# Optimization experiments

Hardware: AMD Instinct MI355X
Metric: run time of the kernel (lower is better)

## Reference

```python
import jax, jax.numpy as jnp
import numpy as np

B_, N, C, H = 512, 49, 256, 8
DH = C // H            # 32
RB, NRF = 8, 32
NWIN = B_ // RB        # 64
DC = 64                # class_token_dim
TC = C + 2 * DC        # 384
WS = 7
SCALE = DH ** -0.5


def _rel_pos_index():
    ch = np.arange(WS)
    coords = np.stack(np.meshgrid(ch, ch, indexing='ij')).reshape(2, -1)  # [2,49]
    rel = (coords[:, :, None] - coords[:, None, :]).transpose(1, 2, 0)    # [49,49,2]
    rel[..., 0] += WS - 1
    rel[..., 1] += WS - 1
    rel[..., 0] *= 2 * WS - 1
    return jnp.asarray(rel.sum(-1).reshape(-1))  # [49*49]


def _ln(x, axes, eps=1e-5):
    m = x.mean(axes, keepdims=True)
    v = x.var(axes, keepdims=True)
    return (x - m) * jax.lax.rsqrt(v + eps)


def setup_inputs() -> dict:
    key = jax.random.key(0)
    ks = jax.random.split(key, 20)
    def w(i, shape, s=0.02):
        return jax.random.normal(ks[i], shape, jnp.float32) * s
    return dict(
        x=w(0, (B_, N, C), 1.0),
        x_ref=w(1, (RB, NRF, C), 1.0),
        depth_token=w(2, (B_, N, DC), 1.0),
        seg_token=w(3, (B_, N, DC), 1.0),
        qkv_w=w(4, (C, 3 * C)), qkv_b=jnp.zeros(3 * C, jnp.float32),
        proj_w=w(5, (C, C)), proj_b=jnp.zeros(C, jnp.float32),
        rel_bias=w(6, ((2 * WS - 1) ** 2, H)),
        diff_mu=w(7, (1, 1, C), 1.0), diff_logsigma=w(8, (1, 1, C)),
        ref_qk_w=w(9, (C, 2 * C)), ref_qk_b=jnp.zeros(2 * C, jnp.float32),
        conv_w=w(10, (H, H, 3, 3), 0.1), conv_b=jnp.zeros(H, jnp.float32),
        q_norm_w=jnp.ones(C, jnp.float32), q_norm_b=jnp.zeros(C, jnp.float32),
        q_proj_w=w(11, (C, C)), q_proj_b=jnp.zeros(C, jnp.float32),
        cls_dth_q_w=w(12, (DC, DC)), cls_dth_q_b=jnp.zeros(DC, jnp.float32),
        cls_seg_q_w=w(13, (DC, DC)), cls_seg_q_b=jnp.zeros(DC, jnp.float32),
        global_k_w=w(14, (TC, TC)), global_k_b=jnp.zeros(TC, jnp.float32),
        global_v_w=w(15, (TC, TC)), global_v_b=jnp.zeros(TC, jnp.float32),
        proj_dth_w=w(16, (DC, DC)), proj_dth_b=jnp.zeros(DC, jnp.float32),
    )


def reference(x, x_ref, depth_token, seg_token, qkv_w, qkv_b, proj_w, proj_b,
              rel_bias, diff_mu, diff_logsigma, ref_qk_w, ref_qk_b, conv_w, conv_b,
              q_norm_w, q_norm_b, q_proj_w, q_proj_b, cls_dth_q_w, cls_dth_q_b,
              cls_seg_q_w, cls_seg_q_b, global_k_w, global_k_b, global_v_w,
              global_v_b, proj_dth_w, proj_dth_b):
    # qkv: [B_,N,3C] -> q,k,v each [B_,H,N,DH]
    qkv = (x @ qkv_w + qkv_b).reshape(B_, N, 3, H, DH).transpose(2, 0, 3, 1, 4)
    q, k, v = qkv[0], qkv[1], qkv[2]

    # ---- group attention (ref branch) ----
    ref_qk = (x_ref @ ref_qk_w + ref_qk_b).reshape(RB, NRF, 2, C).transpose(2, 0, 1, 3)
    ref_q, ref_v = ref_qk[0], ref_qk[1]                       # [RB,NRF,C]
    ref_q = diff_mu + jnp.exp(diff_logsigma) * ref_q
    ref_q = ref_q.reshape(RB, NRF, H, DH).transpose(0, 2, 1, 3)  # [RB,H,NRF,DH]
    ref_v = ref_v.reshape(RB, NRF, H, DH).transpose(0, 2, 1, 3)

    qs = (q * SCALE).reshape(RB, NWIN, H, N, DH)
    # scores against shared (per-image) ref keys; avoids materializing repeated K
    ref_attn = jnp.einsum('rwhnd,rhfd->rhwnf', qs, ref_q)     # [RB,H,NWIN,N,NRF]
    ref_attn_r = ref_attn.reshape(RB, H, NWIN * N, NRF)
    # 3-step diffusion: conv2d over heads-as-channels + LN(no affine) + gelu, residual
    for _ in range(3):
        u = jax.lax.conv_general_dilated(
            ref_attn_r, conv_w, (1, 1), 'SAME',
            dimension_numbers=('NCHW', 'OIHW', 'NCHW')) + conv_b[None, :, None, None]
        u = jax.nn.gelu(_ln(u, (-2, -1)), approximate=False)
        ref_attn_r = ref_attn_r + u
    ref_attn = jax.nn.softmax(ref_attn_r.reshape(RB, H, NWIN, N, NRF), axis=-1)
    q_new = jnp.einsum('rhwnf,rhfd->rwnhd', ref_attn, ref_v).reshape(B_, N, C)
    q_sc = q.transpose(0, 2, 1, 3).reshape(B_, N, C)          # unscaled shortcut
    q_new = (_ln(q_new + q_sc, (-1,)) * q_norm_w + q_norm_b) @ q_proj_w + q_proj_b + q_sc
    q_new = q_new.reshape(B_, N, H, DH).transpose(0, 2, 1, 3) * SCALE

    # ---- window attention with relative position bias ----
    bias = rel_bias[_rel_pos_index()].reshape(N, N, H).transpose(2, 0, 1)  # [H,N,N]
    attn = jax.nn.softmax(jnp.einsum('bhnd,bhmd->bhnm', q_new, k) + bias[None], axis=-1)
    out = jnp.einsum('bhnm,bhmd->bnhd', attn, v).reshape(B_, N, C)
    out = out @ proj_w + proj_b

    # ---- class-token global attention ----
    dch = DC // H   # 8
    tdh = TC // H   # 48
    depth_q = (depth_token @ cls_dth_q_w + cls_dth_q_b).reshape(B_, N, H, dch).transpose(0, 2, 1, 3) * SCALE
    seg_q = (seg_token @ cls_seg_q_w + cls_seg_q_b).reshape(B_, N, H, dch).transpose(0, 2, 1, 3) * SCALE
    t_x = jnp.concatenate([out, depth_token, seg_token], axis=-1)  # [B_,N,TC]
    t_k = (t_x @ global_k_w + global_k_b).reshape(B_, N, H, tdh).transpose(0, 2, 1, 3)
    t_v = (t_x @ global_v_w + global_v_b).reshape(B_, N, H, tdh).transpose(0, 2, 1, 3)

    d_attn = jax.nn.softmax(jnp.einsum('bhnc,bhnt->bhct', depth_q, t_k), axis=-1)
    d_tok = jnp.einsum('bhct,bhnt->bhcn', d_attn, t_v).reshape(B_, DC, N).transpose(0, 2, 1)
    d_tok = d_tok @ proj_dth_w + proj_dth_b
    s_attn = jax.nn.softmax(jnp.einsum('bhnc,bhnt->bhct', seg_q, t_k), axis=-1)
    s_tok = jnp.einsum('bhct,bhnt->bhcn', s_attn, t_v).reshape(B_, DC, N).transpose(0, 2, 1)
    s_tok = s_tok @ proj_dth_w + proj_dth_b  # NOTE: original uses proj_dth for seg too
    return out, d_tok, s_tok
```

## Files before the change

### kernel.cpp

```cpp
#include <hip/hip_runtime.h>
#include <hip/hip_bf16.h>

typedef __hip_bfloat16 bf16;
typedef short s16x8 __attribute__((ext_vector_type(8)));
typedef float f32x4 __attribute__((ext_vector_type(4)));
union V16 { uint4 u4; s16x8 s8; unsigned u[4]; unsigned short s[8]; };

static __device__ __forceinline__ float b2f(bf16 v){ return __bfloat162float(v); }
static __device__ __forceinline__ bf16  f2b(float v){ return __float2bfloat16(v); }
static __device__ __forceinline__ unsigned short f2bs(float x){
    union { float f; unsigned u; } c; c.f = x;
    unsigned r = c.u + 0x7fff + ((c.u >> 16) & 1);
    return (unsigned short)(r >> 16);
}
static __device__ __forceinline__ float bu2f(unsigned short b){
    union { unsigned u; float f; } c; c.u = ((unsigned)b) << 16; return c.f;
}
static __device__ __forceinline__ s16x8 ld16g(const bf16* p){
    V16 u; u.u4 = *(const uint4*)p; return u.s8;
}
static __device__ __forceinline__ void glds16(const void* g, void* l){
    __builtin_amdgcn_global_load_lds(
        (const __attribute__((address_space(1))) unsigned*)g,
        (__attribute__((address_space(3))) unsigned*)l, 16, 0, 0);
}

#define SCALE_T 0.17677669529663687f

__global__ __launch_bounds__(256) void prep_weights(
    const float* __restrict__ qkvw, const float* __restrict__ qpw,
    const float* __restrict__ pw,   const float* __restrict__ gkw,
    const float* __restrict__ gvw,  bf16* __restrict__ Wt)
{
    int idx = blockIdx.x * 256 + threadIdx.x;
    float v;
    if (idx < 196608)      { int j = idx;          int n = j >> 8, k = j & 255; v = qkvw[k * 768 + n]; }
    else if (idx < 262144) { int j = idx - 196608; int n = j >> 8, k = j & 255; v = qpw[k * 256 + n]; }
    else if (idx < 327680) { int j = idx - 262144; int n = j >> 8, k = j & 255; v = pw[k * 256 + n]; }
    else if (idx < 475136) { int j = idx - 327680; int n = j / 384, k = j - n * 384; v = gkw[k * 384 + n]; }
    else                   { int j = idx - 475136; int n = j / 384, k = j - n * 384; v = gvw[k * 384 + n]; }
    ((unsigned short*)Wt)[idx] = f2bs(v);
}

__global__ __launch_bounds__(256) void convert_f32_bf16(
    const float* __restrict__ in, bf16* __restrict__ out)
{
    int i = blockIdx.x * 256 + threadIdx.x;
    float4 v = ((const float4*)in)[i];
    ushort4 o;
    o.x = f2bs(v.x); o.y = f2bs(v.y); o.z = f2bs(v.z); o.w = f2bs(v.w);
    ((ushort4*)out)[i] = o;
}

__global__ __launch_bounds__(256) void tok2b_kernel(
    const float* __restrict__ dth, const float* __restrict__ seg,
    bf16* __restrict__ tokb)
{
    int i = blockIdx.x * 256 + threadIdx.x;
    int row = i >> 4, j8 = i & 15;
    const float* src = (j8 < 8) ? (dth + (size_t)row * 64 + j8 * 8)
                                : (seg + (size_t)row * 64 + (j8 - 8) * 8);
    float4 u0 = ((const float4*)src)[0];
    float4 u1 = ((const float4*)src)[1];
    V16 o;
    o.s[0] = f2bs(u0.x); o.s[1] = f2bs(u0.y);
    o.s[2] = f2bs(u0.z); o.s[3] = f2bs(u0.w);
    o.s[4] = f2bs(u1.x); o.s[5] = f2bs(u1.y);
    o.s[6] = f2bs(u1.z); o.s[7] = f2bs(u1.w);
    *(uint4*)(tokb + (size_t)row * 128 + j8 * 8) = o.u4;
}

template<int TOK>
__global__ __launch_bounds__(256, 4) void gemm_bb(
    const bf16* __restrict__ A, int lda, const bf16* __restrict__ A2,
    const bf16* __restrict__ Wt, const float* __restrict__ bias,
    const float* __restrict__ bias2,
    const bf16* __restrict__ addp, int addStride,
    float* __restrict__ outF, bf16* __restrict__ outB, int outStrideB,
    int K, int N, float scale)
{
    __shared__ char lds[2][16384];

    const int tid = threadIdx.x;
    const int wv = tid >> 6, lane = tid & 63;
    const int quad = lane >> 4, l15 = lane & 15;
    const int wr = wv >> 1, wc = wv & 1;

    const int gx = (int)gridDim.x;
    const int nwg = gx * (int)gridDim.y;
    int bid = (int)blockIdx.y * gx + (int)blockIdx.x;
    if ((nwg & 7) == 0) bid = (bid & 7) * (nwg >> 3) + (bid >> 3);
    const int bx = bid % gx, by = bid / gx;
    const int rowBase = by * 128, colBase = bx * 128;

    const int srow = tid >> 2;
    const int kOffE = (((tid & 3) ^ ((srow >> 1) & 3)) << 3);

    const unsigned swz = (unsigned)((quad ^ ((l15 >> 1) & 3)) << 4);
    const unsigned aoff0 = (unsigned)(wr * 4096 + l15 * 64) + swz;
    const unsigned boff0 = (unsigned)(wc * 4096 + l15 * 64) + swz;

    f32x4 acc[4][4];
    #pragma unroll
    for (int m = 0; m < 4; ++m)
        #pragma unroll
        for (int n = 0; n < 4; ++n)
            #pragma unroll
            for (int r = 0; r < 4; ++r) acc[m][n][r] = 0.f;

    auto stage = [&](int sbuf, int kt) {
        char* base = &lds[sbuf][0];
        #pragma unroll
        for (int c = 0; c < 2; ++c)
            glds16(Wt + (size_t)(colBase + c * 64 + srow) * K + (kt + kOffE),
                   base + 8192 + c * 4096 + tid * 16);
        if (!TOK || kt < 256) {
            #pragma unroll
            for (int c = 0; c < 2; ++c)
                glds16(A + (size_t)(rowBase + c * 64 + srow) * lda + (kt + kOffE),
                       base + c * 4096 + tid * 16);
        } else {
            #pragma unroll
            for (int c = 0; c < 2; ++c)
                glds16(A2 + (size_t)(rowBase + c * 64 + srow) * 128 + (kt - 256 + kOffE),
                       base + c * 4096 + tid * 16);
        }
    };

    stage(0, 0);
    __syncthreads();
    int buf = 0;
    for (int kt = 0; kt < K; kt += 32) {
        if (kt + 32 < K) stage(buf ^ 1, kt + 32);
        const char* Ab2 = &lds[buf][0];
        const char* Bb2 = Ab2 + 8192;
        s16x8 af[4], bfr[4];
        #pragma unroll
        for (int m = 0; m < 4; ++m) af[m]  = *(const s16x8*)(Ab2 + aoff0 + m * 1024);
        #pragma unroll
        for (int n = 0; n < 4; ++n) bfr[n] = *(const s16x8*)(Bb2 + boff0 + n * 1024);
        #pragma unroll
        for (int m = 0; m < 4; ++m)
            #pragma unroll
            for (int n = 0; n < 4; ++n)
                acc[m][n] = __builtin_amdgcn_mfma_f32_16x16x32_bf16(af[m], bfr[n], acc[m][n], 0, 0, 0);
        __syncthreads();
        buf ^= 1;
    }

    if (outB) {
        #pragma unroll
        for (int n = 0; n < 4; ++n) {
            int col = colBase + wc * 64 + n * 16 + l15;
            float bb = bias2 ? (col < 384 ? bias[col] : bias2[col - 384]) : bias[col];
            #pragma unroll
            for (int m = 0; m < 4; ++m) {
                #pragma unroll
                for (int r = 0; r < 4; ++r) {
                    int rl = wr * 64 + m * 16 + quad * 4 + r;
                    float v = acc[m][n][r] + bb;
                    if (addp) v += b2f(addp[(size_t)(rowBase + rl) * addStride + col]);
                    v *= scale;
                    if (outF) outF[(size_t)(rowBase + rl) * N + col] = v;
                    int cbyte = (wc * 64 + n * 16 + l15) * 2;
                    int blk = ((cbyte >> 5) ^ ((rl >> 2) & 7)) & 7;
                    *(unsigned short*)((char*)lds + rl * 256 + (blk << 5) + (cbyte & 31)) = f2bs(v);
                }
            }
        }
        __syncthreads();
        #pragma unroll
        for (int i = 0; i < 8; ++i) {
            int lin = i * 256 + tid;
            int rl = lin >> 4, cb = lin & 15;
            int cb2 = ((((cb >> 1) ^ ((rl >> 2) & 7)) & 7) << 1) | (cb & 1);
            uint4 val = *(const uint4*)((const char*)lds + rl * 256 + cb2 * 16);
            *(uint4*)(outB + (size_t)(rowBase + rl) * outStrideB + colBase + cb * 8) = val;
        }
    } else {
        #pragma unroll
        for (int n = 0; n < 4; ++n) {
            int col = colBase + wc * 64 + n * 16 + l15;
            float bb = bias2 ? (col < 384 ? bias[col] : bias2[col - 384]) : bias[col];
            #pragma unroll
            for (int m = 0; m < 4; ++m) {
                #pragma unroll
                for (int r = 0; r < 4; ++r) {
                    int rl = wr * 64 + m * 16 + quad * 4 + r;
                    float v = acc[m][n][r] + bb;
                    if (addp) v += b2f(addp[(size_t)(rowBase + rl) * addStride + col]);
                    v *= scale;
                    if (outF) outF[(size_t)(rowBase + rl) * N + col] = v;
                }
            }
        }
    }
}

template<int AF32, int OF32>
__global__ __launch_bounds__(256) void small64(
    const void* __restrict__ a0, const void* __restrict__ a1,
    const float* __restrict__ w0, const float* __restrict__ w1,
    const float* __restrict__ b0, const float* __restrict__ b1,
    void* __restrict__ o0, void* __restrict__ o1, float scale)
{
    __shared__ unsigned short WT[64 * 72];
    __shared__ float bsh[64];
    const int task = blockIdx.y;
    const void*  A    = task ? a1 : a0;
    const float* W    = task ? w1 : w0;
    const float* bias = task ? b1 : b0;
    void*        outp = task ? o1 : o0;

    int tid = threadIdx.x;
    for (int l = tid; l < 4096; l += 256) {
        int k = l >> 6, n = l & 63;
        WT[n * 72 + k] = f2bs(W[l]);
    }
    if (tid < 64) bsh[tid] = bias[tid];
    __syncthreads();

    const int wv = tid >> 6, lane = tid & 63;
    const int quad = lane >> 4, l15 = lane & 15;
    const int rowBase = blockIdx.x * 64;
    const int arow = rowBase + wv * 16 + l15;

    s16x8 a[2];
    if (AF32) {
        const float* Ar = (const float*)A + (size_t)arow * 64;
        #pragma unroll
        for (int ks = 0; ks < 2; ++ks) {
            float4 u0 = *(const float4*)(Ar + ks * 32 + quad * 8);
            float4 u1 = *(const float4*)(Ar + ks * 32 + quad * 8 + 4);
            V16 o;
            o.s[0] = f2bs(u0.x); o.s[1] = f2bs(u0.y);
            o.s[2] = f2bs(u0.z); o.s[3] = f2bs(u0.w);
            o.s[4] = f2bs(u1.x); o.s[5] = f2bs(u1.y);
            o.s[6] = f2bs(u1.z); o.s[7] = f2bs(u1.w);
            a[ks] = o.s8;
        }
    } else {
        const bf16* Ar = (const bf16*)A + (size_t)arow * 64;
        #pragma unroll
        for (int ks = 0; ks < 2; ++ks)
            a[ks] = ld16g(Ar + ks * 32 + quad * 8);
    }

    f32x4 acc[4];
    #pragma unroll
    for (int n = 0; n < 4; ++n)
        #pragma unroll
        for (int r = 0; r < 4; ++r) acc[n][r] = 0.f;

    #pragma unroll
    for (int ks = 0; ks < 2; ++ks)
        #pragma unroll
        for (int n = 0; n < 4; ++n) {
            s16x8 b = *(const s16x8*)&WT[(n * 16 + l15) * 72 + ks * 32 + quad * 8];
            acc[n] = __builtin_amdgcn_mfma_f32_16x16x32_bf16(a[ks], b, acc[n], 0, 0, 0);
        }

    #pragma unroll
    for (int n = 0; n < 4; ++n) {
        int col = n * 16 + l15;
        float bb = bsh[col];
        #pragma unroll
        for (int r = 0; r < 4; ++r) {
            int row = rowBase + wv * 16 + quad * 4 + r;
            float v = (acc[n][r] + bb) * scale;
            if (OF32) ((float*)outp)[(size_t)row * 64 + col] = v;
            else      ((bf16*)outp)[(size_t)row * 64 + col] = f2b(v);
        }
    }
}

__global__ __launch_bounds__(256) void mfma_gemm(
    const void* __restrict__ A, int a_mode,
    const float* __restrict__ W, const float* __restrict__ bias,
    float* __restrict__ outF, bf16* __restrict__ outB,
    int M, int K, int N, float scale)
{
    __shared__ __hip_bfloat16 Al[64][48];
    __shared__ __hip_bfloat16 Bl[64][48];

    const int tid  = threadIdx.x;
    const int wv   = tid >> 6, lane = tid & 63;
    const int quad = lane >> 4, l15 = lane & 15;
    const int rowBase = blockIdx.y * 64, colBase = blockIdx.x * 64;

    const int am = tid >> 2, ak = (tid & 3) * 8;
    const int bn = tid & 63, bk = (tid >> 6) * 8;

    f32x4 acc[4];
    #pragma unroll
    for (int t = 0; t < 4; ++t)
        #pragma unroll
        for (int r = 0; r < 4; ++r) acc[t][r] = 0.f;

    for (int kt = 0; kt < K; kt += 32) {
        s16x8 sa;
        if (a_mode == 1) {
            const bf16* Ab = (const bf16*)A;
            V16 u; u.u4 = *(const uint4*)(Ab + (size_t)(rowBase + am) * K + kt + ak);
            sa = u.s8;
        } else {
            const float* src = (const float*)A;
            const float4* p = (const float4*)(src + (size_t)(rowBase + am) * K + kt + ak);
            float4 u0 = p[0], u1 = p[1];
            sa[0] = (short)f2bs(u0.x); sa[1] = (short)f2bs(u0.y);
            sa[2] = (short)f2bs(u0.z); sa[3] = (short)f2bs(u0.w);
            sa[4] = (short)f2bs(u1.x); sa[5] = (short)f2bs(u1.y);
            sa[6] = (short)f2bs(u1.z); sa[7] = (short)f2bs(u1.w);
        }
        *(s16x8*)&Al[am][ak] = sa;

        s16x8 sb;
        #pragma unroll
        for (int j = 0; j < 8; ++j)
            sb[j] = (short)f2bs(W[(size_t)(kt + bk + j) * N + colBase + bn]);
        *(s16x8*)&Bl[bn][bk] = sb;

        __syncthreads();

        s16x8 a = *(const s16x8*)&Al[wv * 16 + l15][quad * 8];
        #pragma unroll
        for (int t = 0; t < 4; ++t) {
            s16x8 b = *(const s16x8*)&Bl[t * 16 + l15][quad * 8];
            acc[t] = __builtin_amdgcn_mfma_f32_16x16x32_bf16(a, b, acc[t], 0, 0, 0);
        }
        __syncthreads();
    }

    #pragma unroll
    for (int t = 0; t < 4; ++t) {
        int col = colBase + t * 16 + l15;
        float bb = bias[col];
        #pragma unroll
        for (int r = 0; r < 4; ++r) {
            int row = rowBase + wv * 16 + quad * 4 + r;
            float v = (acc[t][r] + bb) * scale;
            if (outF) outF[(size_t)row * N + col] = v;
            if (outB) outB[(size_t)row * N + col] = f2b(v);
        }
    }
}

__global__ __launch_bounds__(256) void refprep_kernel(
    const float* __restrict__ ref_qk, const float* __restrict__ mu,
    const float* __restrict__ ls, float* __restrict__ ref_q_t,
    float* __restrict__ ref_v_t)
{
    int idx = blockIdx.x * 256 + threadIdx.x;
    int d = idx & 31, f = (idx >> 5) & 31, h = (idx >> 10) & 7, r = idx >> 13;
    int c = h * 32 + d;
    size_t src = (size_t)(r * 32 + f) * 512 + c;
    ref_q_t[idx] = mu[c] + __expf(ls[c]) * ref_qk[src];
    ref_v_t[idx] = ref_qk[src + 256];
}

__global__ __launch_bounds__(256) void refattn_kernel(
    const bf16* __restrict__ qkv, const float* __restrict__ ref_q_t,
    bf16* __restrict__ ref_attn, float* __restrict__ statsA)
{
    int blk = blockIdx.x;
    int tid = threadIdx.x;
    if (blk == 0 && tid < 384) statsA[tid] = 0.f;
    int w = blk & 63, h = (blk >> 6) & 7, r = blk >> 9;
    int b = r * 64 + w;
    __shared__ float qt[49 * 32];
    __shared__ float rq[32 * 33];
    for (int l = tid; l < 1568; l += 256) {
        int n = l >> 5, d = l & 31;
        qt[l] = b2f(qkv[(size_t)(b * 49 + n) * 768 + h * 32 + d]) * SCALE_T;
    }
    for (int l = tid; l < 1024; l += 256) {
        int f = l >> 5, d = l & 31;
        rq[f * 33 + d] = ref_q_t[(size_t)((r * 8 + h) * 32 + f) * 32 + d];
    }
    __syncthreads();
    for (int l = tid; l < 1568; l += 256) {
        int n = l >> 5, f = l & 31;
        float acc = 0.f;
        #pragma unroll
        for (int d2 = 0; d2 < 32; ++d2) acc += qt[n * 32 + d2] * rq[f * 33 + d2];
        ref_attn[(size_t)(((r * 8 + h) * 64 + w) * 49 + n) * 32 + f] = f2b(acc);
    }
}

__global__ __launch_bounds__(256) void conv_kernel(
    const bf16* __restrict__ in, const float* __restrict__ conv_w,
    const float* __restrict__ conv_b, bf16* __restrict__ u,
    float* __restrict__ statsIt)
{
    __shared__ float w_s[576];
    __shared__ float b_s[8];
    __shared__ float red1[4][8], red2[4][8];
    int tid = threadIdx.x;
    for (int l = tid; l < 576; l += 256) w_s[l] = conv_w[l];
    if (tid < 8) b_s[tid] = conv_b[tid];
    __syncthreads();

    int idx = blockIdx.x * 256 + tid;
    int fb = idx & 3;
    int p  = (idx >> 2) % 3136;
    int r  = idx / 12544;
    int f0 = fb * 8;

    float acc[8][8];
    #pragma unroll
    for (int o = 0; o < 8; ++o) {
        float bo = b_s[o];
        #pragma unroll
        for (int f = 0; f < 8; ++f) acc[o][f] = bo;
    }

    for (int i = 0; i < 8; ++i) {
        float ext[3][10];
        #pragma unroll
        for (int dy = 0; dy < 3; ++dy) {
            int pp = p + dy - 1;
            bool pv = (unsigned)pp < 3136u;
            size_t base = ((size_t)((r * 8 + i) * 3136 + (pv ? pp : 0))) * 32 + f0;
            V16 uv;
            uv.u4 = pv ? *(const uint4*)(in + base) : make_uint4(0, 0, 0, 0);
            #pragma unroll
            for (int j = 0; j < 8; ++j) {
                unsigned sh = uv.u[j >> 1];
                unsigned bits = (j & 1) ? (sh & 0xffff0000u) : (sh << 16);
                union { unsigned uu; float fl; } cv; cv.uu = bits;
                ext[dy][j + 1] = cv.fl;
            }
            ext[dy][0] = (pv && f0 > 0)      ? b2f(in[base - 1]) : 0.f;
            ext[dy][9] = (pv && f0 + 8 < 32) ? b2f(in[base + 8]) : 0.f;
        }
        #pragma unroll
        for (int o = 0; o < 8; ++o) {
            #pragma unroll
            for (int ky = 0; ky < 3; ++ky) {
                const float* wp = &w_s[((o * 8 + i) * 3 + ky) * 3];
                float w0 = wp[0], w1 = wp[1], w2 = wp[2];
                #pragma unroll
                for (int f = 0; f < 8; ++f)
                    acc[o][f] += ext[ky][f] * w0 + ext[ky][f + 1] * w1 + ext[ky][f + 2] * w2;
            }
        }
    }

    float so[8], s2o[8];
    #pragma unroll
    for (int o = 0; o < 8; ++o) {
        bf16 ov[8];
        float s = 0.f, s2 = 0.f;
        #pragma unroll
        for (int f = 0; f < 8; ++f) {
            ov[f] = f2b(acc[o][f]);
            s += acc[o][f]; s2 += acc[o][f] * acc[o][f];
        }
        so[o] = s; s2o[o] = s2;
        *(uint4*)(u + ((size_t)((r * 8 + o) * 3136 + p)) * 32 + f0) = *(uint4*)ov;
    }

    #pragma unroll
    for (int o = 0; o < 8; ++o) {
        #pragma unroll
        for (int off = 32; off > 0; off >>= 1) {
            so[o]  += __shfl_xor(so[o],  off);
            s2o[o] += __shfl_xor(s2o[o], off);
        }
    }
    int wv = tid >> 6, lane = tid & 63;
    if (lane == 0) {
        #pragma unroll
        for (int o = 0; o < 8; ++o) { red1[wv][o] = so[o]; red2[wv][o] = s2o[o]; }
    }
    __syncthreads();
    if (tid < 8) {
        float s = red1[0][tid] + red1[1][tid] + red1[2][tid] + red1[3][tid];
        float s2 = red2[0][tid] + red2[1][tid] + red2[2][tid] + red2[3][tid];
        int g = r * 8 + tid;
        atomicAdd(&statsIt[g * 2], s);
        atomicAdd(&statsIt[g * 2 + 1], s2);
    }
}

__global__ __launch_bounds__(256) void lngelu_kernel(
    const bf16* __restrict__ u, const float* __restrict__ statsIt,
    bf16* __restrict__ ref_attn)
{
    int idx8 = blockIdx.x * 256 + threadIdx.x;
    int g = idx8 / 12544;
    size_t base = (size_t)idx8 * 8;
    float sum = statsIt[g * 2], sq = statsIt[g * 2 + 1];
    float mean = sum * (1.f / 100352.f);
    float var  = sq * (1.f / 100352.f) - mean * mean;
    var = fmaxf(var, 0.f);
    float rstd = rsqrtf(var + 1e-5f);
    V16 uv; uv.u4 = *(const uint4*)(u + base);
    V16 rv; rv.u4 = *(const uint4*)(ref_attn + base);
    bf16 outv[8];
    #pragma unroll
    for (int j = 0; j < 8; ++j) {
        unsigned shu = uv.u[j >> 1];
        unsigned shr = rv.u[j >> 1];
        unsigned bu = (j & 1) ? (shu & 0xffff0000u) : (shu << 16);
        unsigned br = (j & 1) ? (shr & 0xffff0000u) : (shr << 16);
        union { unsigned uu; float fl; } cu, cr; cu.uu = bu; cr.uu = br;
        float v = (cu.fl - mean) * rstd;
        float ge = 0.5f * v * (1.f + erff(v * 0.7071067811865476f));
        outv[j] = f2b(cr.fl + ge);
    }
    *(uint4*)(ref_attn + base) = *(uint4*)outv;
}

__global__ __launch_bounds__(256) void qnew_pre_kernel(
    const bf16* __restrict__ qkv, const bf16* __restrict__ ref_attn,
    const float* __restrict__ ref_v_t,
    const float* __restrict__ qnw, const float* __restrict__ qnb,
    bf16* __restrict__ ln_t)
{
    int ww = threadIdx.x >> 6, lane = threadIdx.x & 63;
    int row = blockIdx.x * 4 + ww;
    int b = row / 49, n = row % 49;
    int r = b >> 6, w = b & 63;
    int h = lane >> 3, d0 = (lane & 7) * 4;

    const bf16* la = ref_attn + ((size_t)(((r * 8 + h) * 64 + w) * 49 + n)) * 32 + d0;
    ushort4 lu = *(const ushort4*)la;
    float lg[4] = { bu2f(lu.x), bu2f(lu.y), bu2f(lu.z), bu2f(lu.w) };

    float m = fmaxf(fmaxf(lg[0], lg[1]), fmaxf(lg[2], lg[3]));
    m = fmaxf(m, __shfl_xor(m, 1));
    m = fmaxf(m, __shfl_xor(m, 2));
    m = fmaxf(m, __shfl_xor(m, 4));
    float p[4], s = 0.f;
    #pragma unroll
    for (int j = 0; j < 4; ++j) { p[j] = __expf(lg[j] - m); s += p[j]; }
    s += __shfl_xor(s, 1);
    s += __shfl_xor(s, 2);
    s += __shfl_xor(s, 4);
    float inv = 1.f / s;
    #pragma unroll
    for (int j = 0; j < 4; ++j) p[j] *= inv;

    const float* rv = ref_v_t + ((size_t)(r * 8 + h) * 32) * 32 + d0;
    float y[4] = {0.f, 0.f, 0.f, 0.f};
    #pragma unroll
    for (int f = 0; f < 32; ++f) {
        int src = (lane & 56) | (f >> 2);
        float pf = __shfl(p[f & 3], src);
        float4 rvf = *(const float4*)(rv + f * 32);
        y[0] += pf * rvf.x; y[1] += pf * rvf.y;
        y[2] += pf * rvf.z; y[3] += pf * rvf.w;
    }

    ushort4 qu = *(const ushort4*)(qkv + (size_t)row * 768 + lane * 4);
    float z[4] = { y[0] + bu2f(qu.x), y[1] + bu2f(qu.y),
                   y[2] + bu2f(qu.z), y[3] + bu2f(qu.w) };

    float s1 = z[0] + z[1] + z[2] + z[3];
    #pragma unroll
    for (int off = 1; off < 64; off <<= 1) s1 += __shfl_xor(s1, off);
    float mean = s1 * (1.f / 256.f);
    float zc[4] = { z[0] - mean, z[1] - mean, z[2] - mean, z[3] - mean };
    float s2 = zc[0]*zc[0] + zc[1]*zc[1] + zc[2]*zc[2] + zc[3]*zc[3];
    #pragma unroll
    for (int off = 1; off < 64; off <<= 1) s2 += __shfl_xor(s2, off);
    float rstd = rsqrtf(s2 * (1.f / 256.f) + 1e-5f);

    float4 wv = *(const float4*)(qnw + lane * 4);
    float4 bv = *(const float4*)(qnb + lane * 4);
    bf16 outv[4];
    outv[0] = f2b(zc[0] * rstd * wv.x + bv.x);
    outv[1] = f2b(zc[1] * rstd * wv.y + bv.y);
    outv[2] = f2b(zc[2] * rstd * wv.z + bv.z);
    outv[3] = f2b(zc[3] * rstd * wv.w + bv.w);
    *(ushort4*)(ln_t + (size_t)row * 256 + lane * 4) = *(ushort4*)outv;
}

__global__ __launch_bounds__(256) void winattn_kernel(
    const bf16* __restrict__ qkv, const bf16* __restrict__ q_new,
    const float* __restrict__ rel_bias, bf16* __restrict__ attn_out)
{
    const int wv = threadIdx.x >> 6, lane = threadIdx.x & 63;
    const int quad = lane >> 4, l15 = lane & 15;
    const int b = blockIdx.x >> 1;
    const int h = (blockIdx.x & 1) * 4 + wv;

    __shared__ bf16 lds[4 * 6912];
    bf16* P  = &lds[wv * 6912];
    bf16* vT = P + 4608;

    {
        int m = lane;
        if (m < 49) {
            const bf16* vp = qkv + ((size_t)(b * 49 + m)) * 768 + 512 + h * 32;
            V16 v0, v1, v2, v3;
            v0.u4 = *(const uint4*)(vp);
            v1.u4 = *(const uint4*)(vp + 8);
            v2.u4 = *(const uint4*)(vp + 16);
            v3.u4 = *(const uint4*)(vp + 24);
            #pragma unroll
            for (int d = 0; d < 8; ++d) {
                ((unsigned short*)vT)[d * 72 + m]        = v0.s[d];
                ((unsigned short*)vT)[(d + 8) * 72 + m]  = v1.s[d];
                ((unsigned short*)vT)[(d + 16) * 72 + m] = v2.s[d];
                ((unsigned short*)vT)[(d + 24) * 72 + m] = v3.s[d];
            }
        } else {
            #pragma unroll
            for (int d = 0; d < 32; ++d)
                ((unsigned short*)vT)[d * 72 + m] = 0;
        }
    }

    s16x8 aq[4], bk[4];
    #pragma unroll
    for (int t = 0; t < 4; ++t) {
        int qr = t * 16 + l15; qr = qr > 48 ? 48 : qr;
        aq[t] = ld16g(q_new + ((size_t)(b * 49 + qr)) * 256 + h * 32 + quad * 8);
        bk[t] = ld16g(qkv + ((size_t)(b * 49 + qr)) * 768 + 256 + h * 32 + quad * 8);
    }
    f32x4 S[4][4];
    #pragma unroll
    for (int tn = 0; tn < 4; ++tn)
        #pragma unroll
        for (int tm = 0; tm < 4; ++tm) {
            #pragma unroll
            for (int r = 0; r < 4; ++r) S[tn][tm][r] = 0.f;
            S[tn][tm] = __builtin_amdgcn_mfma_f32_16x16x32_bf16(aq[tn], bk[tm], S[tn][tm], 0, 0, 0);
        }

    int mvalid[4], mi[4], mj[4];
    #pragma unroll
    for (int tm = 0; tm < 4; ++tm) {
        int m0 = tm * 16 + l15;
        mvalid[tm] = (m0 < 49);
        int mc = m0 > 48 ? 48 : m0;
        mi[tm] = mc / 7; mj[tm] = mc - mi[tm] * 7;
    }
    #pragma unroll
    for (int tn = 0; tn < 4; ++tn) {
        #pragma unroll
        for (int r = 0; r < 4; ++r) {
            int n0 = tn * 16 + quad * 4 + r;
            int nc = n0 > 48 ? 48 : n0;
            int ni = nc / 7, nj = nc - (nc / 7) * 7;
            float vals[4];
            float mx = -1e30f;
            #pragma unroll
            for (int tm = 0; tm < 4; ++tm) {
                float v = S[tn][tm][r]
                        + rel_bias[((ni - mi[tm] + 6) * 13 + (nj - mj[tm] + 6)) * 8 + h];
                if (!mvalid[tm]) v = -1e30f;
                vals[tm] = v;
                mx = fmaxf(mx, v);
            }
            mx = fmaxf(mx, __shfl_xor(mx, 1));
            mx = fmaxf(mx, __shfl_xor(mx, 2));
            mx = fmaxf(mx, __shfl_xor(mx, 4));
            mx = fmaxf(mx, __shfl_xor(mx, 8));
            float s = 0.f;
            #pragma unroll
            for (int tm = 0; tm < 4; ++tm) { vals[tm] = __expf(vals[tm] - mx); s += vals[tm]; }
            s += __shfl_xor(s, 1);
            s += __shfl_xor(s, 2);
            s += __shfl_xor(s, 4);
            s += __shfl_xor(s, 8);
            float inv = 1.f / s;
            #pragma unroll
            for (int tm = 0; tm < 4; ++tm)
                ((unsigned short*)P)[n0 * 72 + tm * 16 + l15] = f2bs(vals[tm] * inv);
        }
    }

    f32x4 O[4][2];
    #pragma unroll
    for (int tn = 0; tn < 4; ++tn)
        #pragma unroll
        for (int td = 0; td < 2; ++td)
            #pragma unroll
            for (int r = 0; r < 4; ++r) O[tn][td][r] = 0.f;

    #pragma unroll
    for (int ks = 0; ks < 2; ++ks) {
        s16x8 bv0 = *(const s16x8*)&vT[(0 * 16 + l15) * 72 + ks * 32 + quad * 8];
        s16x8 bv1 = *(const s16x8*)&vT[(1 * 16 + l15) * 72 + ks * 32 + quad * 8];
        #pragma unroll
        for (int tn = 0; tn < 4; ++tn) {
            s16x8 ap = *(const s16x8*)&P[(tn * 16 + l15) * 72 + ks * 32 + quad * 8];
            O[tn][0] = __builtin_amdgcn_mfma_f32_16x16x32_bf16(ap, bv0, O[tn][0], 0, 0, 0);
            O[tn][1] = __builtin_amdgcn_mfma_f32_16x16x32_bf16(ap, bv1, O[tn][1], 0, 0, 0);
        }
    }

    #pragma unroll
    for (int tn = 0; tn < 4; ++tn)
        #pragma unroll
        for (int r = 0; r < 4; ++r) {
            int n0 = tn * 16 + quad * 4 + r;
            if (n0 < 49) {
                size_t base = ((size_t)(b * 49 + n0)) * 256 + h * 32;
                attn_out[base + l15]      = f2b(O[tn][0][r]);
                attn_out[base + 16 + l15] = f2b(O[tn][1][r]);
            }
        }
}

__global__ __launch_bounds__(256) void clsattn_kernel(
    const bf16* __restrict__ tkv,
    const bf16* __restrict__ depth_q, const bf16* __restrict__ seg_q,
    bf16* __restrict__ d_pre, bf16* __restrict__ s_pre)
{
    const int wv = threadIdx.x >> 6, lane = threadIdx.x & 63;
    const int quad = lane >> 4, l15 = lane & 15;
    const int bh = blockIdx.x * 4 + wv;
    const int b = bh >> 3, h = bh & 7;

    __shared__ bf16 lds[4 * 5760];
    unsigned short* QP = (unsigned short*)&lds[wv * 5760];
    unsigned short* KV = QP + 1152;

    {
        int n = lane;
        V16 dv, sv;
        if (n < 49) {
            dv.u4 = *(const uint4*)(depth_q + ((size_t)(b * 49 + n)) * 64 + h * 8);
            sv.u4 = *(const uint4*)(seg_q   + ((size_t)(b * 49 + n)) * 64 + h * 8);
        } else {
            dv.u4 = make_uint4(0, 0, 0, 0); sv.u4 = make_uint4(0, 0, 0, 0);
        }
        #pragma unroll
        for (int c = 0; c < 8; ++c) {
            QP[c * 72 + n]       = dv.s[c];
            QP[(8 + c) * 72 + n] = sv.s[c];
        }
    }
    {
        int n = lane;
        V16 k[6];
        if (n < 49) {
            const bf16* kp = tkv + ((size_t)(b * 49 + n)) * 768 + h * 48;
            #pragma unroll
            for (int c6 = 0; c6 < 6; ++c6) k[c6].u4 = *(const uint4*)(kp + c6 * 8);
        } else {
            #pragma unroll
            for (int c6 = 0; c6 < 6; ++c6) k[c6].u4 = make_uint4(0, 0, 0, 0);
        }
        #pragma unroll
        for (int c6 = 0; c6 < 6; ++c6)
            #pragma unroll
            for (int j = 0; j < 8; ++j)
                KV[(c6 * 8 + j) * 72 + n] = k[c6].s[j];
    }

    f32x4 S[3];
    #pragma unroll
    for (int t3 = 0; t3 < 3; ++t3)
        #pragma unroll
        for (int r = 0; r < 4; ++r) S[t3][r] = 0.f;
    #pragma unroll
    for (int ks = 0; ks < 2; ++ks) {
        s16x8 a = *(const s16x8*)&QP[l15 * 72 + ks * 32 + quad * 8];
        #pragma unroll
        for (int t3 = 0; t3 < 3; ++t3) {
            s16x8 bf = *(const s16x8*)&KV[(t3 * 16 + l15) * 72 + ks * 32 + quad * 8];
            S[t3] = __builtin_amdgcn_mfma_f32_16x16x32_bf16(a, bf, S[t3], 0, 0, 0);
        }
    }

    #pragma unroll
    for (int r = 0; r < 4; ++r) {
        float v0 = S[0][r], v1 = S[1][r], v2 = S[2][r];
        float mx = fmaxf(fmaxf(v0, v1), v2);
        mx = fmaxf(mx, __shfl_xor(mx, 1));
        mx = fmaxf(mx, __shfl_xor(mx, 2));
        mx = fmaxf(mx, __shfl_xor(mx, 4));
        mx = fmaxf(mx, __shfl_xor(mx, 8));
        float e0 = __expf(v0 - mx), e1 = __expf(v1 - mx), e2 = __expf(v2 - mx);
        float s = e0 + e1 + e2;
        s += __shfl_xor(s, 1);
        s += __shfl_xor(s, 2);
        s += __shfl_xor(s, 4);
        s += __shfl_xor(s, 8);
        float inv = 1.f / s;
        int c = quad * 4 + r;
        QP[c * 72 + 0 * 16 + l15] = f2bs(e0 * inv);
        QP[c * 72 + 1 * 16 + l15] = f2bs(e1 * inv);
        QP[c * 72 + 2 * 16 + l15] = f2bs(e2 * inv);
    }
    #pragma unroll
    for (int z = 0; z < 4; ++z)
        QP[(lane & 15) * 72 + 48 + (lane >> 4) * 4 + z] = 0;

    {
        int n = lane;
        V16 v[6], zv; zv.u4 = make_uint4(0, 0, 0, 0);
        if (n < 49) {
            const bf16* vp = tkv + ((size_t)(b * 49 + n)) * 768 + 384 + h * 48;
            #pragma unroll
            for (int c6 = 0; c6 < 6; ++c6) v[c6].u4 = *(const uint4*)(vp + c6 * 8);
        } else {
            #pragma unroll
            for (int c6 = 0; c6 < 6; ++c6) v[c6].u4 = zv.u4;
        }
        #pragma unroll
        for (int c6 = 0; c6 < 6; ++c6)
            *(uint4*)&KV[n * 72 + c6 * 8] = v[c6].u4;
        *(uint4*)&KV[n * 72 + 48] = zv.u4;
        *(uint4*)&KV[n * 72 + 56] = zv.u4;
    }

    f32x4 O[4];
    #pragma unroll
    for (int t4 = 0; t4 < 4; ++t4)
        #pragma unroll
        for (int r = 0; r < 4; ++r) O[t4][r] = 0.f;
    #pragma unroll
    for (int ks = 0; ks < 2; ++ks) {
        s16x8 a = *(const s16x8*)&QP[l15 * 72 + ks * 32 + quad * 8];
        #pragma unroll
        for (int t4 = 0; t4 < 4; ++t4) {
            s16x8 bf = *(const s16x8*)&KV[(t4 * 16 + l15) * 72 + ks * 32 + quad * 8];
            O[t4] = __builtin_amdgcn_mfma_f32_16x16x32_bf16(a, bf, O[t4], 0, 0, 0);
        }
    }

    #pragma unroll
    for (int t4 = 0; t4 < 4; ++t4) {
        int n = t4 * 16 + l15;
        if (n < 49) {
            size_t base = ((size_t)(b * 49 + n)) * 64 + h * 8;
            #pragma unroll
            for (int r = 0; r < 4; ++r) {
                int c = quad * 4 + r;
                if (c < 8) d_pre[base + c] = f2b(O[t4][r]);
                else       s_pre[base + c - 8] = f2b(O[t4][r]);
            }
        }
    }
}

extern "C" void kernel_launch(void* const* d_in, const int* in_sizes, int n_in,
                              void* d_out, int out_size, void* d_ws, size_t ws_size,
                              hipStream_t stream)
{
    const float* x          = (const float*)d_in[0];
    const float* x_ref      = (const float*)d_in[1];
    const float* dth_tok    = (const float*)d_in[2];
    const float* seg_tok    = (const float*)d_in[3];
    const float* qkv_w      = (const float*)d_in[4];
    const float* qkv_b      = (const float*)d_in[5];
    const float* proj_w     = (const float*)d_in[6];
    const float* proj_b     = (const float*)d_in[7];
    const float* rel_bias   = (const float*)d_in[8];
    const float* diff_mu    = (const float*)d_in[9];
    const float* diff_ls    = (const float*)d_in[10];
    const float* ref_qk_w   = (const float*)d_in[11];
    const float* ref_qk_b   = (const float*)d_in[12];
    const float* conv_w     = (const float*)d_in[13];
    const float* conv_b     = (const float*)d_in[14];
    const float* q_norm_w   = (const float*)d_in[15];
    const float* q_norm_b   = (const float*)d_in[16];
    const float* q_proj_w   = (const float*)d_in[17];
    const float* q_proj_b   = (const float*)d_in[18];
    const float* cls_dth_w  = (const float*)d_in[19];
    const float* cls_dth_b  = (const float*)d_in[20];
    const float* cls_seg_w  = (const float*)d_in[21];
    const float* cls_seg_b  = (const float*)d_in[22];
    const float* glob_k_w   = (const float*)d_in[23];
    const float* glob_k_b   = (const float*)d_in[24];
    const float* glob_v_w   = (const float*)d_in[25];
    const float* glob_v_b   = (const float*)d_in[26];
    const float* proj_dth_w = (const float*)d_in[27];
    const float* proj_dth_b = (const float*)d_in[28];

    bf16* wsb = (bf16*)d_ws;
    bf16* qkv      = wsb;
    bf16* tkv      = wsb;
    bf16* ref_attn = wsb + 19267584;
    bf16* q_new    = ref_attn;
    bf16* out0b    = ref_attn;
    bf16* depth_q  = ref_attn;
    bf16* seg_q    = ref_attn + 1605632;
    bf16* d_pre    = ref_attn + 3211264;
    bf16* s_pre    = ref_attn + 4816896;
    bf16* u_buf    = wsb + 25690112;
    bf16* xb       = u_buf;
    bf16* ln_t     = u_buf;
    bf16* attn_out = u_buf;
    float* ref_qk  = (float*)((char*)d_ws + 64225280);
    float* ref_q_t = ref_qk + 131072;
    float* ref_v_t = ref_q_t + 65536;
    float* statsA  = ref_qk;

    float* out0  = (float*)d_out;
    float* out_d = out0 + 6422528;
    float* out_s = out0 + 8028160;

    bf16* Wt_all = (bf16*)out_d;
    bf16* tokb   = (bf16*)out_s;

    prep_weights<<<2432, 256, 0, stream>>>(qkv_w, q_proj_w, proj_w, glob_k_w, glob_v_w, Wt_all);
    convert_f32_bf16<<<6272, 256, 0, stream>>>(x, xb);
    tok2b_kernel<<<1568, 256, 0, stream>>>(dth_tok, seg_tok, tokb);

    gemm_bb<0><<<dim3(6, 196), 256, 0, stream>>>(xb, 256, nullptr,
        Wt_all, qkv_b, nullptr, nullptr, 0, nullptr, qkv, 768, 256, 768, 1.f);
    mfma_gemm<<<dim3(8, 4), 256, 0, stream>>>(x_ref, 0, ref_qk_w, ref_qk_b,
                                              ref_qk, nullptr, 256, 256, 512, 1.f);
    refprep_kernel<<<256, 256, 0, stream>>>(ref_qk, diff_mu, diff_ls, ref_q_t, ref_v_t);
    refattn_kernel<<<4096, 256, 0, stream>>>(qkv, ref_q_t, ref_attn, statsA);
    for (int it = 0; it < 3; ++it) {
        conv_kernel<<<392, 256, 0, stream>>>(ref_attn, conv_w, conv_b, u_buf, statsA + it * 128);
        lngelu_kernel<<<3136, 256, 0, stream>>>(u_buf, statsA + it * 128, ref_attn);
    }
    qnew_pre_kernel<<<6272, 256, 0, stream>>>(qkv, ref_attn, ref_v_t,
                                              q_norm_w, q_norm_b, ln_t);
    gemm_bb<0><<<dim3(2, 196), 256, 0, stream>>>(ln_t, 256, nullptr,
        Wt_all + 196608, q_proj_b, nullptr, qkv, 768, nullptr, q_new, 256, 256, 256, SCALE_T);
    winattn_kernel<<<1024, 256, 0, stream>>>(qkv, q_new, rel_bias, attn_out);
    gemm_bb<0><<<dim3(2, 196), 256, 0, stream>>>(attn_out, 256, nullptr,
        Wt_all + 262144, proj_b, nullptr, nullptr, 0, out0, out0b, 256, 256, 256, 1.f);
    gemm_bb<1><<<dim3(6, 196), 256, 0, stream>>>(out0b, 256, tokb,
        Wt_all + 327680, glob_k_b, glob_v_b, nullptr, 0, nullptr, tkv, 768, 384, 768, 1.f);
    small64<1, 0><<<dim3(392, 2), 256, 0, stream>>>(dth_tok, seg_tok,
        cls_dth_w, cls_seg_w, cls_dth_b, cls_seg_b, depth_q, seg_q, SCALE_T);
    clsattn_kernel<<<1024, 256, 0, stream>>>(tkv, depth_q, seg_q, d_pre, s_pre);
    small64<0, 1><<<dim3(392, 2), 256, 0, stream>>>(d_pre, s_pre,
        proj_dth_w, proj_dth_w, proj_dth_b, proj_dth_b, out_d, out_s, 1.f);
}
```

Baseline: 517.2 us.

## Deepen GEMM LDS pipeline to four stages; move LN stats to separate kernel

The bf16 GEMM now keeps four LDS buffers and prefetches three k-steps ahead. It waits with explicit vmcnt and one barrier per step, replacing two-buffer double buffering with a sync after every step. Occupancy drops to 2 blocks per SM in exchange for hiding more global-load latency. The conv kernel also no longer does per-block reductions with atomics for layer-norm statistics; a new lnstats kernel instead reduces each quarter-group deterministically. This adds an extra pass over u_buf on each of the three iterations.

Result: faster. 496.3 us (-4.0%).

```diff
diff --git a/kernel.cpp b/kernel.cpp
--- a/kernel.cpp
+++ b/kernel.cpp
@@ -71,7 +71,7 @@
 }
 
 template<int TOK>
-__global__ __launch_bounds__(256, 4) void gemm_bb(
+__global__ __launch_bounds__(256, 2) void gemm_pipe(
     const bf16* __restrict__ A, int lda, const bf16* __restrict__ A2,
     const bf16* __restrict__ Wt, const float* __restrict__ bias,
     const float* __restrict__ bias2,
@@ -79,7 +79,7 @@
     float* __restrict__ outF, bf16* __restrict__ outB, int outStrideB,
     int K, int N, float scale)
 {
-    __shared__ char lds[2][16384];
+    __shared__ char lds[4][16384];
 
     const int tid = threadIdx.x;
     const int wv = tid >> 6, lane = tid & 63;
@@ -108,8 +108,11 @@
             #pragma unroll
             for (int r = 0; r < 4; ++r) acc[m][n][r] = 0.f;
 
-    auto stage = [&](int sbuf, int kt) {
-        char* base = &lds[sbuf][0];
+    const int nsteps = K >> 5;
+
+    auto stageN = [&](int i) {
+        int kt = i << 5;
+        char* base = &lds[i & 3][0];
         #pragma unroll
         for (int c = 0; c < 2; ++c)
             glds16(Wt + (size_t)(colBase + c * 64 + srow) * K + (kt + kOffE),
@@ -127,12 +130,22 @@
         }
     };
 
-    stage(0, 0);
-    __syncthreads();
-    int buf = 0;
-    for (int kt = 0; kt < K; kt += 32) {
-        if (kt + 32 < K) stage(buf ^ 1, kt + 32);
-        const char* Ab2 = &lds[buf][0];
+    stageN(0);
+    if (nsteps > 1) stageN(1);
+    if (nsteps > 2) stageN(2);
+
+    for (int i = 0; i < nsteps; ++i) {
+        int a = nsteps - 1 - i; if (a > 2) a = 2;
+        if (a == 2)      asm volatile("s_waitcnt vmcnt(8)" ::: "memory");
+        else if (a == 1) asm volatile("s_waitcnt vmcnt(4)" ::: "memory");
+        else             asm volatile("s_waitcnt vmcnt(0)" ::: "memory");
+        __builtin_amdgcn_sched_barrier(0);
+        __builtin_amdgcn_s_barrier();
+        __builtin_amdgcn_sched_barrier(0);
+
+        if (i + 3 < nsteps) stageN(i + 3);
+
+        const char* Ab2 = &lds[i & 3][0];
         const char* Bb2 = Ab2 + 8192;
         s16x8 af[4], bfr[4];
         #pragma unroll
@@ -144,8 +157,6 @@
             #pragma unroll
             for (int n = 0; n < 4; ++n)
                 acc[m][n] = __builtin_amdgcn_mfma_f32_16x16x32_bf16(af[m], bfr[n], acc[m][n], 0, 0, 0);
-        __syncthreads();
-        buf ^= 1;
     }
 
     if (outB) {
@@ -360,15 +371,14 @@
 
 __global__ __launch_bounds__(256) void refattn_kernel(
     const bf16* __restrict__ qkv, const float* __restrict__ ref_q_t,
-    bf16* __restrict__ ref_attn, float* __restrict__ statsA)
+    bf16* __restrict__ ref_attn)
 {
     int blk = blockIdx.x;
-    int tid = threadIdx.x;
-    if (blk == 0 && tid < 384) statsA[tid] = 0.f;
     int w = blk & 63, h = (blk >> 6) & 7, r = blk >> 9;
     int b = r * 64 + w;
     __shared__ float qt[49 * 32];
     __shared__ float rq[32 * 33];
+    int tid = threadIdx.x;
     for (int l = tid; l < 1568; l += 256) {
         int n = l >> 5, d = l & 31;
         qt[l] = b2f(qkv[(size_t)(b * 49 + n) * 768 + h * 32 + d]) * SCALE_T;
@@ -389,12 +399,10 @@
 
 __global__ __launch_bounds__(256) void conv_kernel(
     const bf16* __restrict__ in, const float* __restrict__ conv_w,
-    const float* __restrict__ conv_b, bf16* __restrict__ u,
-    float* __restrict__ statsIt)
+    const float* __restrict__ conv_b, bf16* __restrict__ u)
 {
     __shared__ float w_s[576];
     __shared__ float b_s[8];
-    __shared__ float red1[4][8], red2[4][8];
     int tid = threadIdx.x;
     for (int l = tid; l < 576; l += 256) w_s[l] = conv_w[l];
     if (tid < 8) b_s[tid] = conv_b[tid];
@@ -446,51 +454,57 @@
         }
     }
 
-    float so[8], s2o[8];
     #pragma unroll
     for (int o = 0; o < 8; ++o) {
         bf16 ov[8];
-        float s = 0.f, s2 = 0.f;
-        #pragma unroll
-        for (int f = 0; f < 8; ++f) {
-            ov[f] = f2b(acc[o][f]);
-            s += acc[o][f]; s2 += acc[o][f] * acc[o][f];
-        }
-        so[o] = s; s2o[o] = s2;
+        #pragma unroll
+        for (int f = 0; f < 8; ++f) ov[f] = f2b(acc[o][f]);
         *(uint4*)(u + ((size_t)((r * 8 + o) * 3136 + p)) * 32 + f0) = *(uint4*)ov;
     }
-
-    #pragma unroll
-    for (int o = 0; o < 8; ++o) {
-        #pragma unroll
-        for (int off = 32; off > 0; off >>= 1) {
-            so[o]  += __shfl_xor(so[o],  off);
-            s2o[o] += __shfl_xor(s2o[o], off);
-        }
-    }
-    int wv = tid >> 6, lane = tid & 63;
-    if (lane == 0) {
-        #pragma unroll
-        for (int o = 0; o < 8; ++o) { red1[wv][o] = so[o]; red2[wv][o] = s2o[o]; }
-    }
-    __syncthreads();
-    if (tid < 8) {
-        float s = red1[0][tid] + red1[1][tid] + red1[2][tid] + red1[3][tid];
-        float s2 = red2[0][tid] + red2[1][tid] + red2[2][tid] + red2[3][tid];
-        int g = r * 8 + tid;
-        atomicAdd(&statsIt[g * 2], s);
-        atomicAdd(&statsIt[g * 2 + 1], s2);
+}
+
+__global__ __launch_bounds__(256) void lnstats_kernel(
+    const bf16* __restrict__ u, float* __restrict__ stats4)
+{
+    int g4 = blockIdx.x;
+    const bf16* p = u + (size_t)g4 * 25088;
+    int tid = threadIdx.x;
+    float s = 0.f, s2 = 0.f;
+    for (int it = tid; it < 3136; it += 256) {
+        V16 uv; uv.u4 = *(const uint4*)(p + it * 8);
+        #pragma unroll
+        for (int j = 0; j < 8; ++j) {
+            unsigned sh = uv.u[j >> 1];
+            unsigned bits = (j & 1) ? (sh & 0xffff0000u) : (sh << 16);
+            union { unsigned uu; float fl; } cv; cv.uu = bits;
+            s += cv.fl; s2 += cv.fl * cv.fl;
+        }
+    }
+    __shared__ float r1[256], r2[256];
+    r1[tid] = s; r2[tid] = s2; __syncthreads();
+    for (int st = 128; st > 0; st >>= 1) {
+        if (tid < st) { r1[tid] += r1[tid + st]; r2[tid] += r2[tid + st]; }
+        __syncthreads();
+    }
+    if (tid == 0) {
+        stats4[g4 * 2]     = r1[0];
+        stats4[g4 * 2 + 1] = r2[0];
     }
 }
 
 __global__ __launch_bounds__(256) void lngelu_kernel(
-    const bf16* __restrict__ u, const float* __restrict__ statsIt,
+    const bf16* __restrict__ u, const float* __restrict__ stats4,
     bf16* __restrict__ ref_attn)
 {
     int idx8 = blockIdx.x * 256 + threadIdx.x;
     int g = idx8 / 12544;
     size_t base = (size_t)idx8 * 8;
-    float sum = statsIt[g * 2], sq = statsIt[g * 2 + 1];
+    float sum = 0.f, sq = 0.f;
+    #pragma unroll
+    for (int q = 0; q < 4; ++q) {
+        sum += stats4[(g * 4 + q) * 2];
+        sq  += stats4[(g * 4 + q) * 2 + 1];
+    }
     float mean = sum * (1.f / 100352.f);
     float var  = sq * (1.f / 100352.f) - mean * mean;
     var = fmaxf(var, 0.f);
@@ -891,7 +905,7 @@
     float* ref_qk  = (float*)((char*)d_ws + 64225280);
     float* ref_q_t = ref_qk + 131072;
     float* ref_v_t = ref_q_t + 65536;
-    float* statsA  = ref_qk;
+    float* stats4  = ref_qk;
 
     float* out0  = (float*)d_out;
     float* out_d = out0 + 6422528;
@@ -904,24 +918,25 @@
     convert_f32_bf16<<<6272, 256, 0, stream>>>(x, xb);
     tok2b_kernel<<<1568, 256, 0, stream>>>(dth_tok, seg_tok, tokb);
 
-    gemm_bb<0><<<dim3(6, 196), 256, 0, stream>>>(xb, 256, nullptr,
+    gemm_pipe<0><<<dim3(6, 196), 256, 0, stream>>>(xb, 256, nullptr,
         Wt_all, qkv_b, nullptr, nullptr, 0, nullptr, qkv, 768, 256, 768, 1.f);
     mfma_gemm<<<dim3(8, 4), 256, 0, stream>>>(x_ref, 0, ref_qk_w, ref_qk_b,
                                               ref_qk, nullptr, 256, 256, 512, 1.f);
     refprep_kernel<<<256, 256, 0, stream>>>(ref_qk, diff_mu, diff_ls, ref_q_t, ref_v_t);
-    refattn_kernel<<<4096, 256, 0, stream>>>(qkv, ref_q_t, ref_attn, statsA);
+    refattn_kernel<<<4096, 256, 0, stream>>>(qkv, ref_q_t, ref_attn);
     for (int it = 0; it < 3; ++it) {
-        conv_kernel<<<392, 256, 0, stream>>>(ref_attn, conv_w, conv_b, u_buf, statsA + it * 128);
-        lngelu_kernel<<<3136, 256, 0, stream>>>(u_buf, statsA + it * 128, ref_attn);
+        conv_kernel<<<392, 256, 0, stream>>>(ref_attn, conv_w, conv_b, u_buf);
+        lnstats_kernel<<<256, 256, 0, stream>>>(u_buf, stats4);
+        lngelu_kernel<<<3136, 256, 0, stream>>>(u_buf, stats4, ref_attn);
     }
     qnew_pre_kernel<<<6272, 256, 0, stream>>>(qkv, ref_attn, ref_v_t,
                                               q_norm_w, q_norm_b, ln_t);
-    gemm_bb<0><<<dim3(2, 196), 256, 0, stream>>>(ln_t, 256, nullptr,
+    gemm_pipe<0><<<dim3(2, 196), 256, 0, stream>>>(ln_t, 256, nullptr,
         Wt_all + 196608, q_proj_b, nullptr, qkv, 768, nullptr, q_new, 256, 256, 256, SCALE_T);
     winattn_kernel<<<1024, 256, 0, stream>>>(qkv, q_new, rel_bias, attn_out);
-    gemm_bb<0><<<dim3(2, 196), 256, 0, stream>>>(attn_out, 256, nullptr,
+    gemm_pipe<0><<<dim3(2, 196), 256, 0, stream>>>(attn_out, 256, nullptr,
         Wt_all + 262144, proj_b, nullptr, nullptr, 0, out0, out0b, 256, 256, 256, 1.f);
-    gemm_bb<1><<<dim3(6, 196), 256, 0, stream>>>(out0b, 256, tokb,
+    gemm_pipe<1><<<dim3(6, 196), 256, 0, stream>>>(out0b, 256, tokb,
         Wt_all + 327680, glob_k_b, glob_v_b, nullptr, 0, nullptr, tkv, 768, 384, 768, 1.f);
     small64<1, 0><<<dim3(392, 2), 256, 0, stream>>>(dth_tok, seg_tok,
         cls_dth_w, cls_seg_w, cls_dth_b, cls_seg_b, depth_q, seg_q, SCALE_T);
```
